# Kernel tuning notes

Measured on AMD Instinct MI355X. Metric: run time of the kernel, lower is better.

The kernel has to match this reference:

```python
import jax, jax.numpy as jnp
import numpy as np

N_TIME, N_BATCH, N_STATE, N_FORCE = 64, 8192, 32, 16
DT = 0.05          # implicit (backward-Euler) step size
NEWTON_ITERS = 6   # fixed Newton-Raphson iteration count (converges well below fp32 eps here)


def setup_inputs() -> dict:
    key = jax.random.key(0)
    k = jax.random.split(key, 5)
    return {
        "y0": jax.random.normal(k[0], (N_BATCH, N_STATE), jnp.float32) * 0.1,
        "forces": jax.random.normal(k[1], (N_TIME, N_BATCH, N_FORCE), jnp.float32),
        "W": jax.random.normal(k[2], (N_STATE, N_STATE), jnp.float32) / np.float32(np.sqrt(N_STATE)),
        "U": jax.random.normal(k[3], (N_STATE, N_FORCE), jnp.float32) / np.float32(np.sqrt(N_FORCE)),
        "b": jax.random.normal(k[4], (N_STATE,), jnp.float32) * 0.01,
        "n": N_TIME,
    }


def reference(y0, forces, W, U, b, n):
    """Sequential recursive nonlinear solve, block_size=1, ZeroPredictor guess.

    Each step solves R(y_k) = y_k - y_{k-1} - dt*tanh(W y_k + U u_k + b) = 0
    via Newton-Raphson with a batched dense solve of the diagonal Jacobian
    block J[1] = I - dt*diag(1-t^2) W (the Thomas factorization for a single
    step reduces to this dense solve).
    """
    S = y0.shape[-1]
    I = jnp.eye(S, dtype=y0.dtype)

    def step(y_prev, u):
        fu = u @ U.T + b                      # [B,S] constant per Newton solve
        y = jnp.zeros_like(y_prev)            # ZeroPredictor initial guess
        for _ in range(NEWTON_ITERS):         # plain Newton-Raphson
            t = jnp.tanh(y @ W.T + fu)        # [B,S]
            R = y - y_prev - DT * t           # residual [B,S]
            J = I - DT * ((1.0 - t * t)[..., :, None] * W)  # [B,S,S] dR/dy
            y = y - jnp.linalg.solve(J, R[..., None])[..., 0]
        return y, y

    _, ys = jax.lax.scan(step, y0, forces[1:n])   # sequential recursion over time
    return jnp.concatenate([y0[None], ys], axis=0)  # result[0] = y0
```

## Files before the change

kernel.cpp:

```cpp
#include <hip/hip_runtime.h>

#define NT 64
#define NB 8192
#define NS 32
#define NF 16
#define DT 0.05f
#define FP_ITERS 3
#define YSTR 36

typedef float f32x2 __attribute__((ext_vector_type(2)));
typedef float f32x4 __attribute__((ext_vector_type(4)));

__device__ __forceinline__ f32x2 tanh2(f32x2 x) {
    const float K = 2.8853900817779268f;
    float e0 = __builtin_amdgcn_exp2f(K * x[0]);
    float e1 = __builtin_amdgcn_exp2f(K * x[1]);
    float r0 = __builtin_amdgcn_rcpf(e0 + 1.0f);
    float r1 = __builtin_amdgcn_rcpf(e1 + 1.0f);
    f32x2 r;
    r[0] = fmaf(-2.0f, r0, 1.0f);
    r[1] = fmaf(-2.0f, r1, 1.0f);
    return r;
}

__global__ __launch_bounds__(256, 2) void rnes_kernel(
    const float* __restrict__ y0,
    const float* __restrict__ forces,
    const float* __restrict__ W,
    const float* __restrict__ U,
    const float* __restrict__ bias,
    float* __restrict__ out)
{
    const int lane = threadIdx.x & 63;
    const int wv   = threadIdx.x >> 6;
    const int b    = lane >> 4;
    const int p    = lane & 15;
    const int batch = blockIdx.x * 16 + wv * 4 + b;

    __shared__ __align__(16) float Ysh[4][4 * YSTR];
    float* Yw = Ysh[wv] + b * YSTR;

    f32x2 W2[NS];
#pragma unroll
    for (int k = 0; k < NS; k += 4) {
        f32x4 r0 = *(const f32x4*)(W + (2*p)   * NS + k);
        f32x4 r1 = *(const f32x4*)(W + (2*p+1) * NS + k);
#pragma unroll
        for (int e = 0; e < 4; ++e) W2[k+e] = (f32x2){r0[e], r1[e]};
    }
    f32x2 U2[NF];
#pragma unroll
    for (int f = 0; f < NF; f += 4) {
        f32x4 r0 = *(const f32x4*)(U + (2*p)   * NF + f);
        f32x4 r1 = *(const f32x4*)(U + (2*p+1) * NF + f);
#pragma unroll
        for (int e = 0; e < 4; ++e) U2[f+e] = (f32x2){r0[e], r1[e]};
    }
    const f32x2 b2 = *(const f32x2*)(bias + 2*p);

    f32x2 yp = *(const f32x2*)(y0 + (size_t)batch * NS + 2*p);
    __builtin_nontemporal_store(yp, (f32x2*)(out + (size_t)batch * NS + 2*p));
    *(f32x2*)(Yw + 2*p) = yp;
    asm volatile("" ::: "memory");

    const size_t fstep = (size_t)NB * NF;
    const f32x4* fb = (const f32x4*)(forces + (size_t)batch * NF);
    f32x4 upf[4];
#pragma unroll
    for (int j = 0; j < 4; ++j)
        upf[j] = __builtin_nontemporal_load(&fb[(fstep >> 2) + j]);

    for (int k = 1; k < NT; ++k) {
        f32x2 a0 = b2, a1 = (f32x2){0.f, 0.f};
#pragma unroll
        for (int f = 0; f < NF; f += 4) {
            f32x4 u4 = upf[f >> 2];
            a0 = U2[f+0] * u4[0] + a0;
            a1 = U2[f+1] * u4[1] + a1;
            a0 = U2[f+2] * u4[2] + a0;
            a1 = U2[f+3] * u4[3] + a1;
        }
        const f32x2 fu = a0 + a1;

        {
            int kn = (k + 1 < NT) ? (k + 1) : (NT - 1);
#pragma unroll
            for (int j = 0; j < 4; ++j)
                upf[j] = __builtin_nontemporal_load(&fb[(size_t)kn * (fstep >> 2) + j]);
        }

        f32x2 y = yp;
#pragma unroll
        for (int it = 0; it < FP_ITERS; ++it) {
            f32x2 z0 = fu, z1 = (f32x2){0.f, 0.f};
#pragma unroll
            for (int i = 0; i < 8; ++i) {
                f32x4 yv = ((const f32x4*)Yw)[i];
                z0 = W2[4*i+0] * yv[0] + z0;
                z1 = W2[4*i+1] * yv[1] + z1;
                z0 = W2[4*i+2] * yv[2] + z0;
                z1 = W2[4*i+3] * yv[3] + z1;
            }
            f32x2 t = tanh2(z0 + z1);
            y[0] = fmaf(DT, t[0], yp[0]);
            y[1] = fmaf(DT, t[1], yp[1]);
            asm volatile("" ::: "memory");
            *(f32x2*)(Yw + 2*p) = y;
            asm volatile("" ::: "memory");
        }

        yp = y;
        __builtin_nontemporal_store(y, (f32x2*)(out + ((size_t)k * NB + batch) * NS + 2*p));
    }
}

extern "C" void kernel_launch(void* const* d_in, const int* in_sizes, int n_in,
                              void* d_out, int out_size, void* d_ws, size_t ws_size,
                              hipStream_t stream) {
    const float* y0     = (const float*)d_in[0];
    const float* forces = (const float*)d_in[1];
    const float* W      = (const float*)d_in[2];
    const float* U      = (const float*)d_in[3];
    const float* b      = (const float*)d_in[4];
    float* out = (float*)d_out;

    dim3 grid(NB / 16);
    dim3 block(256);
    rnes_kernel<<<grid, block, 0, stream>>>(y0, forces, W, U, b, out);
}
```

Measured before the change: 165.0 us.

## Split state matvec across two half-waves with ds_swizzle reduction

Each batch element now gets 32 lanes instead of 16. The two 16-lane halves each compute half of the W·y and U·u dot products, and the partial sums are combined with a ds_swizzle xor-16 exchange before the tanh. This halves the per-thread register footprint for W and U and shortens the serial FMA chain in each fixed-point iteration. Launch bounds go to 4 blocks per CU and the grid doubles to keep the same total work. In exchange it adds a cross-lane exchange per iteration, redundant shared-memory writes from the second half, and twice as many threads doing the tanh.

```diff
diff --git a/kernel.cpp b/kernel.cpp
--- a/kernel.cpp
+++ b/kernel.cpp
@@ -6,7 +6,7 @@
 #define NF 16
 #define DT 0.05f
 #define FP_ITERS 3
-#define YSTR 36
+#define YROW 72
 
 typedef float f32x2 __attribute__((ext_vector_type(2)));
 typedef float f32x4 __attribute__((ext_vector_type(4)));
@@ -23,7 +23,14 @@
     return r;
 }
 
-__global__ __launch_bounds__(256, 2) void rnes_kernel(
+__device__ __forceinline__ f32x2 swz16(f32x2 v) {
+    f32x2 r;
+    r[0] = __int_as_float(__builtin_amdgcn_ds_swizzle(__float_as_int(v[0]), 0x401F));
+    r[1] = __int_as_float(__builtin_amdgcn_ds_swizzle(__float_as_int(v[1]), 0x401F));
+    return r;
+}
+
+__global__ __launch_bounds__(256, 4) void rnes_kernel(
     const float* __restrict__ y0,
     const float* __restrict__ forces,
     const float* __restrict__ W,
@@ -33,84 +40,89 @@
 {
     const int lane = threadIdx.x & 63;
     const int wv   = threadIdx.x >> 6;
-    const int b    = lane >> 4;
+    const int b    = lane >> 5;
+    const int h    = (lane >> 4) & 1;
     const int p    = lane & 15;
-    const int batch = blockIdx.x * 16 + wv * 4 + b;
+    const int batch = blockIdx.x * 8 + wv * 2 + b;
 
-    __shared__ __align__(16) float Ysh[4][4 * YSTR];
-    float* Yw = Ysh[wv] + b * YSTR;
+    __shared__ __align__(16) float Ysh[4][2 * YROW];
+    float* Yw = Ysh[wv] + b * YROW;
+    float* Ywr = Yw + h * 36;
 
-    f32x2 W2[NS];
+    f32x2 W2[16];
 #pragma unroll
-    for (int k = 0; k < NS; k += 4) {
-        f32x4 r0 = *(const f32x4*)(W + (2*p)   * NS + k);
-        f32x4 r1 = *(const f32x4*)(W + (2*p+1) * NS + k);
+    for (int c = 0; c < 16; c += 4) {
+        f32x4 r0 = *(const f32x4*)(W + (2*p)   * NS + h*16 + c);
+        f32x4 r1 = *(const f32x4*)(W + (2*p+1) * NS + h*16 + c);
 #pragma unroll
-        for (int e = 0; e < 4; ++e) W2[k+e] = (f32x2){r0[e], r1[e]};
+        for (int e = 0; e < 4; ++e) W2[c+e] = (f32x2){r0[e], r1[e]};
     }
-    f32x2 U2[NF];
+    f32x2 U2[8];
 #pragma unroll
-    for (int f = 0; f < NF; f += 4) {
-        f32x4 r0 = *(const f32x4*)(U + (2*p)   * NF + f);
-        f32x4 r1 = *(const f32x4*)(U + (2*p+1) * NF + f);
+    for (int c = 0; c < 8; c += 4) {
+        f32x4 r0 = *(const f32x4*)(U + (2*p)   * NF + h*8 + c);
+        f32x4 r1 = *(const f32x4*)(U + (2*p+1) * NF + h*8 + c);
 #pragma unroll
-        for (int e = 0; e < 4; ++e) U2[f+e] = (f32x2){r0[e], r1[e]};
+        for (int e = 0; e < 4; ++e) U2[c+e] = (f32x2){r0[e], r1[e]};
     }
-    const f32x2 b2 = *(const f32x2*)(bias + 2*p);
+    f32x2 bh = (f32x2){0.f, 0.f};
+    if (h == 0) bh = *(const f32x2*)(bias + 2*p);
 
     f32x2 yp = *(const f32x2*)(y0 + (size_t)batch * NS + 2*p);
-    __builtin_nontemporal_store(yp, (f32x2*)(out + (size_t)batch * NS + 2*p));
-    *(f32x2*)(Yw + 2*p) = yp;
+    if (h == 0)
+        __builtin_nontemporal_store(yp, (f32x2*)(out + (size_t)batch * NS + 2*p));
+    *(f32x2*)(Ywr + 2*p) = yp;
     asm volatile("" ::: "memory");
 
-    const size_t fstep = (size_t)NB * NF;
-    const f32x4* fb = (const f32x4*)(forces + (size_t)batch * NF);
-    f32x4 upf[4];
-#pragma unroll
-    for (int j = 0; j < 4; ++j)
-        upf[j] = __builtin_nontemporal_load(&fb[(fstep >> 2) + j]);
+    const size_t f4step = (size_t)NB * NF / 4;
+    const f32x4* fb = (const f32x4*)(forces + (size_t)batch * NF) + h * 2;
+    f32x4 u0 = __builtin_nontemporal_load(fb + f4step);
+    f32x4 u1 = __builtin_nontemporal_load(fb + f4step + 1);
 
     for (int k = 1; k < NT; ++k) {
-        f32x2 a0 = b2, a1 = (f32x2){0.f, 0.f};
-#pragma unroll
-        for (int f = 0; f < NF; f += 4) {
-            f32x4 u4 = upf[f >> 2];
-            a0 = U2[f+0] * u4[0] + a0;
-            a1 = U2[f+1] * u4[1] + a1;
-            a0 = U2[f+2] * u4[2] + a0;
-            a1 = U2[f+3] * u4[3] + a1;
-        }
+        f32x2 a0 = bh, a1 = (f32x2){0.f, 0.f};
+        a0 = U2[0] * u0[0] + a0;
+        a1 = U2[1] * u0[1] + a1;
+        a0 = U2[2] * u0[2] + a0;
+        a1 = U2[3] * u0[3] + a1;
+        a0 = U2[4] * u1[0] + a0;
+        a1 = U2[5] * u1[1] + a1;
+        a0 = U2[6] * u1[2] + a0;
+        a1 = U2[7] * u1[3] + a1;
         const f32x2 fu = a0 + a1;
 
         {
             int kn = (k + 1 < NT) ? (k + 1) : (NT - 1);
-#pragma unroll
-            for (int j = 0; j < 4; ++j)
-                upf[j] = __builtin_nontemporal_load(&fb[(size_t)kn * (fstep >> 2) + j]);
+            u0 = __builtin_nontemporal_load(fb + (size_t)kn * f4step);
+            u1 = __builtin_nontemporal_load(fb + (size_t)kn * f4step + 1);
         }
 
         f32x2 y = yp;
 #pragma unroll
         for (int it = 0; it < FP_ITERS; ++it) {
             f32x2 z0 = fu, z1 = (f32x2){0.f, 0.f};
+            const f32x4* Yr = (const f32x4*)(Yw + h * 16);
 #pragma unroll
-            for (int i = 0; i < 8; ++i) {
-                f32x4 yv = ((const f32x4*)Yw)[i];
+            for (int i = 0; i < 4; ++i) {
+                f32x4 yv = Yr[i];
                 z0 = W2[4*i+0] * yv[0] + z0;
                 z1 = W2[4*i+1] * yv[1] + z1;
                 z0 = W2[4*i+2] * yv[2] + z0;
                 z1 = W2[4*i+3] * yv[3] + z1;
             }
-            f32x2 t = tanh2(z0 + z1);
+            f32x2 z = z0 + z1;
+            f32x2 zt = z + swz16(z);
+            f32x2 t = tanh2(zt);
             y[0] = fmaf(DT, t[0], yp[0]);
             y[1] = fmaf(DT, t[1], yp[1]);
             asm volatile("" ::: "memory");
-            *(f32x2*)(Yw + 2*p) = y;
+            *(f32x2*)(Ywr + 2*p) = y;
             asm volatile("" ::: "memory");
         }
 
         yp = y;
-        __builtin_nontemporal_store(y, (f32x2*)(out + ((size_t)k * NB + batch) * NS + 2*p));
+        if (h == 0)
+            __builtin_nontemporal_store(y, (f32x2*)(out + ((size_t)k * NB + batch) * NS + 2*p));
     }
 }
 
@@ -124,7 +136,7 @@
     const float* b      = (const float*)d_in[4];
     float* out = (float*)d_out;
 
-    dim3 grid(NB / 16);
+    dim3 grid(NB / 8);
     dim3 block(256);
     rnes_kernel<<<grid, block, 0, stream>>>(y0, forces, W, U, b, out);
 }
```

After: 174.0 us. 1.05x slower.

## Replace LDS state broadcast with DPP row-rotate ring matvec

Applied to the files above, without the earlier changes.

Each lane's state values are now passed around the 16-lane row with DPP row_ror shifts instead of being written to shared memory and read back as vectors. This removes the LDS store/load round trip from the serial fixed-point loop. The W entries are pre-permuted into registers to match the rotation order, and the rotation direction is detected at runtime. In exchange it adds 30 DPP moves per iteration and uses more registers for the split W arrays.

```diff
diff --git a/kernel.cpp b/kernel.cpp
--- a/kernel.cpp
+++ b/kernel.cpp
@@ -6,7 +6,6 @@
 #define NF 16
 #define DT 0.05f
 #define FP_ITERS 3
-#define YSTR 36
 
 typedef float f32x2 __attribute__((ext_vector_type(2)));
 typedef float f32x4 __attribute__((ext_vector_type(4)));
@@ -23,6 +22,11 @@
     return r;
 }
 
+__device__ __forceinline__ float ror1f(float v) {
+    return __int_as_float(__builtin_amdgcn_update_dpp(
+        0, __float_as_int(v), 0x121, 0xF, 0xF, true));
+}
+
 __global__ __launch_bounds__(256, 2) void rnes_kernel(
     const float* __restrict__ y0,
     const float* __restrict__ forces,
@@ -37,17 +41,17 @@
     const int p    = lane & 15;
     const int batch = blockIdx.x * 16 + wv * 4 + b;
 
-    __shared__ __align__(16) float Ysh[4][4 * YSTR];
-    float* Yw = Ysh[wv] + b * YSTR;
+    const int got = __builtin_amdgcn_update_dpp(0, p, 0x121, 0xF, 0xF, true) & 15;
+    const int dir = (got == ((p + 1) & 15)) ? 1 : 15;
 
-    f32x2 W2[NS];
+    f32x2 Wa[16], Wb[16];
 #pragma unroll
-    for (int k = 0; k < NS; k += 4) {
-        f32x4 r0 = *(const f32x4*)(W + (2*p)   * NS + k);
-        f32x4 r1 = *(const f32x4*)(W + (2*p+1) * NS + k);
-#pragma unroll
-        for (int e = 0; e < 4; ++e) W2[k+e] = (f32x2){r0[e], r1[e]};
+    for (int j = 0; j < 16; ++j) {
+        const int q = (p + dir * j) & 15;
+        Wa[j] = (f32x2){ W[(2*p) * NS + 2*q],     W[(2*p+1) * NS + 2*q]     };
+        Wb[j] = (f32x2){ W[(2*p) * NS + 2*q + 1], W[(2*p+1) * NS + 2*q + 1] };
     }
+
     f32x2 U2[NF];
 #pragma unroll
     for (int f = 0; f < NF; f += 4) {
@@ -60,8 +64,6 @@
 
     f32x2 yp = *(const f32x2*)(y0 + (size_t)batch * NS + 2*p);
     __builtin_nontemporal_store(yp, (f32x2*)(out + (size_t)batch * NS + 2*p));
-    *(f32x2*)(Yw + 2*p) = yp;
-    asm volatile("" ::: "memory");
 
     const size_t fstep = (size_t)NB * NF;
     const f32x4* fb = (const f32x4*)(forces + (size_t)batch * NF);
@@ -93,20 +95,16 @@
 #pragma unroll
         for (int it = 0; it < FP_ITERS; ++it) {
             f32x2 z0 = fu, z1 = (f32x2){0.f, 0.f};
+            float yc0 = y[0], yc1 = y[1];
 #pragma unroll
-            for (int i = 0; i < 8; ++i) {
-                f32x4 yv = ((const f32x4*)Yw)[i];
-                z0 = W2[4*i+0] * yv[0] + z0;
-                z1 = W2[4*i+1] * yv[1] + z1;
-                z0 = W2[4*i+2] * yv[2] + z0;
-                z1 = W2[4*i+3] * yv[3] + z1;
+            for (int j = 0; j < 16; ++j) {
+                z0 = Wa[j] * yc0 + z0;
+                z1 = Wb[j] * yc1 + z1;
+                if (j < 15) { yc0 = ror1f(yc0); yc1 = ror1f(yc1); }
             }
             f32x2 t = tanh2(z0 + z1);
             y[0] = fmaf(DT, t[0], yp[0]);
             y[1] = fmaf(DT, t[1], yp[1]);
-            asm volatile("" ::: "memory");
-            *(f32x2*)(Yw + 2*p) = y;
-            asm volatile("" ::: "memory");
         }
 
         yp = y;
```

Measured after the change: 190.5 us. +15.4%, slower.
